# Kernel optimization log

Measured on AMD Instinct MI355X. Metric: run time of the kernel, lower is better.

The kernel has to match this reference:

```python
import jax, jax.numpy as jnp
import numpy as np
import math

DIM = 512
HEADS = 8
K_SEEDS = 4
HEAD_DIM = DIM // HEADS
EPS = 1e-6


def setup_inputs() -> dict:
    key = jax.random.key(0)
    ks = jax.random.split(key, 12)
    B, N = 16, 8192
    s = 1.0 / math.sqrt(DIM)
    inp = {
        "X": jax.random.normal(ks[0], (B, N, DIM), dtype=jnp.float32),
        "seed": jax.random.normal(ks[1], (1, K_SEEDS, DIM), dtype=jnp.float32),
        "Wq": jax.random.uniform(ks[2], (DIM, DIM), minval=-s, maxval=s),
        "bq": jax.random.uniform(ks[3], (DIM,), minval=-s, maxval=s),
        "Wk": jax.random.uniform(ks[4], (DIM, DIM), minval=-s, maxval=s),
        "bk": jax.random.uniform(ks[5], (DIM,), minval=-s, maxval=s),
        "Wv": jax.random.uniform(ks[6], (DIM, DIM), minval=-s, maxval=s),
        "bv": jax.random.uniform(ks[7], (DIM,), minval=-s, maxval=s),
        "Wo": jax.random.uniform(ks[8], (DIM, DIM), minval=-s, maxval=s),
        "bo": jax.random.uniform(ks[9], (DIM,), minval=-s, maxval=s),
        "gamma": jnp.ones((DIM,), dtype=jnp.float32),
        "beta": jnp.zeros((DIM,), dtype=jnp.float32),
    }
    return inp


def reference(X, seed, Wq, bq, Wk, bk, Wv, bv, Wo, bo, gamma, beta):
    B, N, _ = X.shape
    S = jnp.broadcast_to(seed, (B, K_SEEDS, DIM))  # expanded seed vectors
    # QKV projections (torch Linear: x @ W.T + b)
    q = (S @ Wq.T + bq).reshape(B, K_SEEDS, HEADS, HEAD_DIM)
    k = (X @ Wk.T + bk).reshape(B, N, HEADS, HEAD_DIM)
    v = (X @ Wv.T + bv).reshape(B, N, HEADS, HEAD_DIM)
    # scores: [B, H, Kq, N]
    scores = jnp.einsum("bqhd,bnhd->bhqn", q, k) / math.sqrt(HEAD_DIM)
    attn = jax.nn.softmax(scores, axis=-1)
    out = jnp.einsum("bhqn,bnhd->bqhd", attn, v).reshape(B, K_SEEDS, DIM)
    out = out @ Wo.T + bo
    # residual + LayerNorm
    h = out + S
    mu = jnp.mean(h, axis=-1, keepdims=True)
    var = jnp.mean((h - mu) ** 2, axis=-1, keepdims=True)
    return (h - mu) * jax.lax.rsqrt(var + EPS) * gamma + beta
```

## Files before the change

kernel.cpp:

```cpp
#include <hip/hip_runtime.h>
#include <math.h>

#define DIM 512
#define KQn 4
#define HQ  32
#define BB  16
#define NN  8192
#define EPSLN 1e-6f
#define TROWS  32

typedef _Float16 f16;
typedef _Float16 h2_t __attribute__((ext_vector_type(2)));
typedef __fp16   g2_t __attribute__((ext_vector_type(2)));
typedef _Float16 h8_t __attribute__((ext_vector_type(8)));
typedef float    f32x4 __attribute__((ext_vector_type(4)));

union U32H2 { unsigned int u; h2_t h; g2_t g; };
union U4H8  { uint4 u; h8_t h; unsigned int w[4]; };

__device__ inline unsigned int pkh2(float a, float b) {
    U32H2 v; v.g = __builtin_amdgcn_cvt_pkrtz(a, b); return v.u;
}
__device__ inline h2_t ash2(unsigned int u) { U32H2 v; v.u = u; return v.h; }

#if __has_builtin(__builtin_amdgcn_fdot2)
__device__ inline float fdot2f(unsigned int a, unsigned int b, float c) {
    return __builtin_amdgcn_fdot2(ash2(a), ash2(b), c, false);
}
#else
__device__ inline float fdot2f(unsigned int a, unsigned int b, float c) {
    h2_t ha = ash2(a), hb = ash2(b);
    return c + (float)ha.x*(float)hb.x + (float)ha.y*(float)hb.y;
}
#endif

__global__ __launch_bounds__(256) void k_q(
    const float* __restrict__ seed, const float* __restrict__ Wq,
    const float* __restrict__ bq, float* __restrict__ q_g)
{
    int hq = blockIdx.x; int h = hq >> 2; int j = hq & 3;
    int t = threadIdx.x;
    __shared__ float qpart[256];
    int d = t >> 2, q4 = t & 3;
    const float* sr = seed + j*DIM + q4*128;
    const float* wr = Wq + (size_t)(h*64 + d)*DIM + q4*128;
    float acc = 0.f;
    for (int c = 0; c < 128; c += 4) {
        float4 s4 = *(const float4*)(sr + c);
        float4 w4 = *(const float4*)(wr + c);
        acc += s4.x*w4.x + s4.y*w4.y + s4.z*w4.z + s4.w*w4.w;
    }
    qpart[t] = acc;
    __syncthreads();
    if (t < 64)
        q_g[hq*64 + t] = qpart[t*4] + qpart[t*4+1] + qpart[t*4+2] + qpart[t*4+3] + bq[h*64 + t];
}

__global__ __launch_bounds__(256) void k_qk(
    const float* __restrict__ Wk, const float* __restrict__ q_g, f16* __restrict__ qkB)
{
    const int h = blockIdx.x;
    const int cs = blockIdx.y;
    const int t = threadIdx.x;
    __shared__ float q_s[4][64];
    __shared__ float red2[4][128];
    q_s[t >> 6][t & 63] = q_g[(h*4 + (t >> 6))*64 + (t & 63)];
    __syncthreads();
    const int c = cs*128 + (t & 127);
    const int dh = t >> 7;
    float a0=0.f, a1=0.f, a2=0.f, a3=0.f;
    const float* wb = Wk + ((size_t)(h*64 + dh*32))*DIM + c;
    #pragma unroll 8
    for (int d = 0; d < 32; ++d) {
        float w = wb[(size_t)d*DIM];
        a0 += q_s[0][dh*32 + d]*w;
        a1 += q_s[1][dh*32 + d]*w;
        a2 += q_s[2][dh*32 + d]*w;
        a3 += q_s[3][dh*32 + d]*w;
    }
    if (dh == 1) {
        red2[0][t & 127] = a0; red2[1][t & 127] = a1;
        red2[2][t & 127] = a2; red2[3][t & 127] = a3;
    }
    __syncthreads();
    if (dh == 0) {
        int ci = t & 127;
        float v[4];
        v[0] = (a0 + red2[0][ci]) * 0.125f;
        v[1] = (a1 + red2[1][ci]) * 0.125f;
        v[2] = (a2 + red2[2][ci]) * 0.125f;
        v[3] = (a3 + red2[3][ci]) * 0.125f;
        const int kb = c >> 5, g = (c >> 3) & 3, ii = c & 7;
        #pragma unroll
        for (int j = 0; j < 4; ++j) {
            const int hq = h*4 + j;
            const int nb = hq >> 4, lane = g*16 + (hq & 15);
            qkB[(((size_t)(kb*2 + nb)*64 + lane) << 3) + ii] = (f16)v[j];
        }
    }
}

__global__ __launch_bounds__(256, 4) void k_att(
    const float* __restrict__ X, const f16* __restrict__ qkB,
    f16* __restrict__ opart, float* __restrict__ lpart,
    int nchunk, int crows, int ntile)
{
    const int chunk = blockIdx.x, b = blockIdx.y;
    const int t = threadIdx.x;

    __shared__ f16 Xcm[512][36];
    __shared__ f16 p_s[32][36];
    __shared__ float lred[256];

    unsigned int* XcmU = (unsigned int*)&Xcm[0][0];
    unsigned int* pW   = (unsigned int*)&p_s[0][0];

    const int w    = t >> 6;
    const int lane = t & 63;
    const int mb = w & 1, nb = w >> 1;
    const int lg = lane >> 4;
    const int lm = lane & 15;

    const int rp = t >> 4;
    const int cq = (t & 15) << 1;

    const int hg = t >> 5;
    const int cg = t & 31;

    float o_acc[4][16];
    #pragma unroll
    for (int j = 0; j < 4; ++j)
        #pragma unroll
        for (int i = 0; i < 16; ++i) o_acc[j][i] = 0.f;
    float l_local = 0.f;

    const size_t xbase = (size_t)b*NN*DIM;
    const uint4* qkB4 = (const uint4*)qkB;

    for (int tile = 0; tile < ntile; ++tile) {
        const int r0 = chunk*crows + tile*TROWS;
        __syncthreads();
        {
            const float2* Xr0 = (const float2*)(X + xbase + (size_t)(r0 + rp*2    )*DIM);
            const float2* Xr1 = (const float2*)(X + xbase + (size_t)(r0 + rp*2 + 1)*DIM);
            #pragma unroll
            for (int cs = 0; cs < 16; ++cs) {
                int c0 = cs*32 + cq;
                float2 xa = Xr0[c0 >> 1];
                float2 xb = Xr1[c0 >> 1];
                XcmU[c0*18 + rp]     = pkh2(xa.x, xb.x);
                XcmU[(c0+1)*18 + rp] = pkh2(xa.y, xb.y);
            }
        }
        {
            const float* xr = X + xbase + (size_t)(r0 + mb*16 + lm)*DIM + lg*8;
            f32x4 acc0 = {0.f,0.f,0.f,0.f}, acc1 = {0.f,0.f,0.f,0.f};
            #pragma unroll
            for (int kb = 0; kb < 16; ++kb) {
                float4 a0 = *(const float4*)(xr + kb*32);
                float4 a1 = *(const float4*)(xr + kb*32 + 4);
                U4H8 af;
                af.w[0] = pkh2(a0.x, a0.y); af.w[1] = pkh2(a0.z, a0.w);
                af.w[2] = pkh2(a1.x, a1.y); af.w[3] = pkh2(a1.z, a1.w);
                U4H8 bf; bf.u = qkB4[(size_t)(kb*2 + nb)*64 + lane];
                if (kb & 1) acc1 = __builtin_amdgcn_mfma_f32_16x16x32_f16(af.h, bf.h, acc1, 0, 0, 0);
                else        acc0 = __builtin_amdgcn_mfma_f32_16x16x32_f16(af.h, bf.h, acc0, 0, 0, 0);
            }
            float p0 = __expf(fminf(acc0[0] + acc1[0], 30.f));
            float p1 = __expf(fminf(acc0[1] + acc1[1], 30.f));
            float p2 = __expf(fminf(acc0[2] + acc1[2], 30.f));
            float p3 = __expf(fminf(acc0[3] + acc1[3], 30.f));
            l_local += p0 + p1 + p2 + p3;
            const int pidx = (nb*16 + lm)*18 + mb*8 + lg*2;
            pW[pidx]     = pkh2(p0, p1);
            pW[pidx + 1] = pkh2(p2, p3);
        }
        __syncthreads();
        {
            const unsigned int* pU = (const unsigned int*)&p_s[0][0];
            #pragma unroll
            for (int ng = 0; ng < 4; ++ng) {
                unsigned int pd[4][4];
                #pragma unroll
                for (int j = 0; j < 4; ++j) {
                    uint2 pa = *(const uint2*)&pU[(hg*4 + j)*18 + ng*4];
                    uint2 pb = *(const uint2*)&pU[(hg*4 + j)*18 + ng*4 + 2];
                    pd[j][0] = pa.x; pd[j][1] = pa.y; pd[j][2] = pb.x; pd[j][3] = pb.y;
                }
                #pragma unroll
                for (int mm = 0; mm < 4; ++mm) {
                    #pragma unroll
                    for (int cc = 0; cc < 4; ++cc) {
                        const int c = cg + mm*32 + cc*128;
                        const int ci = mm*4 + cc;
                        const unsigned int* row = &XcmU[c*18 + ng*4];
                        uint2 xa = *(const uint2*)&row[0];
                        uint2 xb = *(const uint2*)&row[2];
                        #pragma unroll
                        for (int j = 0; j < 4; ++j) {
                            float a = o_acc[j][ci];
                            a = fdot2f(pd[j][0], xa.x, a);
                            a = fdot2f(pd[j][1], xa.y, a);
                            a = fdot2f(pd[j][2], xb.x, a);
                            a = fdot2f(pd[j][3], xb.y, a);
                            o_acc[j][ci] = a;
                        }
                    }
                }
            }
        }
    }
    __syncthreads();
    lred[w*64 + lane] = l_local;
    __syncthreads();
    if (t < 32) {
        const int nb2 = t >> 4, col = t & 15;
        float l = 0.f;
        #pragma unroll
        for (int mm = 0; mm < 2; ++mm)
            #pragma unroll
            for (int g = 0; g < 4; ++g)
                l += lred[(nb2*2 + mm)*64 + g*16 + col];
        lpart[((size_t)b*nchunk + chunk)*HQ + t] = l;
    }
    const size_t obase = (((size_t)b*nchunk + chunk)*HQ + hg*4)*DIM + cg;
    #pragma unroll
    for (int j = 0; j < 4; ++j)
        #pragma unroll
        for (int mm = 0; mm < 4; ++mm)
            #pragma unroll
            for (int cc = 0; cc < 4; ++cc)
                opart[obase + (size_t)j*DIM + mm*32 + cc*128] = (f16)o_acc[j][mm*4 + cc];
}

__global__ __launch_bounds__(256) void k_red(
    const f16* __restrict__ opart, const float* __restrict__ lpart,
    const float* __restrict__ Wv, const float* __restrict__ bv,
    float* __restrict__ vbuf, int nchunk)
{
    const int hq = blockIdx.x, b = blockIdx.y;
    const int h = hq >> 2, j = hq & 3;
    const int t = threadIdx.x;
    __shared__ float pool_s[512];
    __shared__ float ls[64];
    __shared__ float linv_s;
    if (t < nchunk) ls[t] = lpart[((size_t)b*nchunk + t)*HQ + hq];
    __syncthreads();
    if (t == 0) {
        float l = 0.f;
        for (int i = 0; i < nchunk; ++i) l += ls[i];
        linv_s = 1.f / l;
    }
    float a0 = 0.f, a1 = 0.f;
    const unsigned int* opU = (const unsigned int*)opart;
    #pragma unroll 4
    for (int ch = 0; ch < nchunk; ++ch) {
        unsigned int u = opU[((((size_t)b*nchunk + ch)*HQ + hq) << 8) + t];
        h2_t hv = ash2(u);
        a0 += (float)hv.x; a1 += (float)hv.y;
    }
    __syncthreads();
    float linv = linv_s;
    pool_s[2*t]   = a0 * linv;
    pool_s[2*t+1] = a1 * linv;
    __syncthreads();
    const int o1 = t >> 2, q4 = t & 3;
    const float* wr = Wv + ((size_t)(h*64 + o1))*DIM + q4*128;
    const float* ps = pool_s + q4*128;
    float acc = 0.f;
    #pragma unroll 8
    for (int c = 0; c < 128; c += 4) {
        float4 w4 = *(const float4*)(wr + c);
        float4 p4 = *(const float4*)(ps + c);
        acc += w4.x*p4.x + w4.y*p4.y + w4.z*p4.z + w4.w*p4.w;
    }
    acc += __shfl_xor(acc, 1);
    acc += __shfl_xor(acc, 2);
    if (q4 == 0)
        vbuf[((size_t)b*KQn + j)*DIM + h*64 + o1] = acc + bv[h*64 + o1];
}

__global__ __launch_bounds__(512) void k_wo_ln(
    const float* __restrict__ vbuf, const float* __restrict__ Wo, const float* __restrict__ bo,
    const float* __restrict__ seed, const float* __restrict__ gamma, const float* __restrict__ beta,
    float* __restrict__ out)
{
    const int j = blockIdx.x, b = blockIdx.y;
    const int t = threadIdx.x;
    __shared__ float v_s[512];
    __shared__ float wsum[8], wsq[8];
    v_s[t] = vbuf[((size_t)b*KQn + j)*DIM + t];
    __syncthreads();
    const float* wr = Wo + (size_t)t*DIM;
    float acc = bo[t];
    #pragma unroll 8
    for (int c = 0; c < 512; c += 4) {
        float4 w4 = *(const float4*)(wr + c);
        float4 p4 = *(const float4*)&v_s[c];
        acc += w4.x*p4.x + w4.y*p4.y + w4.z*p4.z + w4.w*p4.w;
    }
    float hv = acc + seed[j*DIM + t];
    float s1 = hv, s2 = hv*hv;
    #pragma unroll
    for (int m = 1; m <= 32; m <<= 1) {
        s1 += __shfl_xor(s1, m);
        s2 += __shfl_xor(s2, m);
    }
    if ((t & 63) == 0) { wsum[t >> 6] = s1; wsq[t >> 6] = s2; }
    __syncthreads();
    float tm = 0.f, tq = 0.f;
    #pragma unroll
    for (int i = 0; i < 8; ++i) { tm += wsum[i]; tq += wsq[i]; }
    float mu = tm * (1.f/512.f);
    float var = tq * (1.f/512.f) - mu*mu;
    float rs = rsqrtf(var + EPSLN);
    out[((size_t)b*KQn + j)*DIM + t] = (hv - mu)*rs*gamma[t] + beta[t];
}

extern "C" void kernel_launch(void* const* d_in, const int* in_sizes, int n_in,
                              void* d_out, int out_size, void* d_ws, size_t ws_size,
                              hipStream_t stream) {
    const float* X     = (const float*)d_in[0];
    const float* seed  = (const float*)d_in[1];
    const float* Wq    = (const float*)d_in[2];
    const float* bq    = (const float*)d_in[3];
    const float* Wk    = (const float*)d_in[4];
    const float* Wv    = (const float*)d_in[6];
    const float* bv    = (const float*)d_in[7];
    const float* Wo    = (const float*)d_in[8];
    const float* bo    = (const float*)d_in[9];
    const float* gamma = (const float*)d_in[10];
    const float* beta  = (const float*)d_in[11];

    int nchunk = 64;
    {
        const size_t need64 = 303104UL + (size_t)BB*64*HQ*DIM*2;
        if (ws_size < need64) nchunk = 32;
    }
    const int crows = NN / nchunk;
    const int ntile = crows / TROWS;

    char* ws = (char*)d_ws;
    float* q_g   = (float*)(ws + 0);
    f16*   qkB   = (f16*)  (ws + 8192);
    size_t off_lpart = 40960;
    size_t off_vbuf  = off_lpart + (size_t)BB*nchunk*HQ*4;
    size_t off_opart = off_vbuf + (size_t)BB*KQn*DIM*4;
    float* lpart = (float*)(ws + off_lpart);
    float* vbuf  = (float*)(ws + off_vbuf);
    f16*   opart = (f16*)  (ws + off_opart);
    float* out   = (float*)d_out;

    k_q    <<<32,               256, 0, stream>>>(seed, Wq, bq, q_g);
    k_qk   <<<dim3(8, 4),       256, 0, stream>>>(Wk, q_g, qkB);
    k_att  <<<dim3(nchunk, BB), 256, 0, stream>>>(X, qkB, opart, lpart, nchunk, crows, ntile);
    k_red  <<<dim3(HQ, BB),     256, 0, stream>>>(opart, lpart, Wv, bv, vbuf, nchunk);
    k_wo_ln<<<dim3(KQn, BB),    512, 0, stream>>>(vbuf, Wo, bo, seed, gamma, beta, out);
}
```

Measured before the change: 555.7 us.

## Use MFMA for attention-weighted X accumulation instead of fdot2 loops

Replaces the scalar fdot2-based P·X accumulation in k_att with 16x16x32 f16 MFMA instructions, reading P fragments from a re-padded shared buffer and X column-major fragments from Xcm. Partial outputs are staged through shared memory and written out with coalesced 16-byte stores instead of scattered f16 stores. k_red's chunk-sum of the softmax denominators becomes a wavefront shuffle reduction instead of a serial loop. This should cut the VALU work in the main loop, in exchange for more complex fragment indexing and extra LDS traffic for the output transpose.

```diff
diff --git a/kernel.cpp b/kernel.cpp
--- a/kernel.cpp
+++ b/kernel.cpp
@@ -22,17 +22,6 @@
     U32H2 v; v.g = __builtin_amdgcn_cvt_pkrtz(a, b); return v.u;
 }
 __device__ inline h2_t ash2(unsigned int u) { U32H2 v; v.u = u; return v.h; }
-
-#if __has_builtin(__builtin_amdgcn_fdot2)
-__device__ inline float fdot2f(unsigned int a, unsigned int b, float c) {
-    return __builtin_amdgcn_fdot2(ash2(a), ash2(b), c, false);
-}
-#else
-__device__ inline float fdot2f(unsigned int a, unsigned int b, float c) {
-    h2_t ha = ash2(a), hb = ash2(b);
-    return c + (float)ha.x*(float)hb.x + (float)ha.y*(float)hb.y;
-}
-#endif
 
 __global__ __launch_bounds__(256) void k_q(
     const float* __restrict__ seed, const float* __restrict__ Wq,
@@ -109,7 +98,7 @@
     const int t = threadIdx.x;
 
     __shared__ f16 Xcm[512][36];
-    __shared__ f16 p_s[32][36];
+    __shared__ f16 p_s[32][40];
     __shared__ float lred[256];
 
     unsigned int* XcmU = (unsigned int*)&Xcm[0][0];
@@ -124,14 +113,13 @@
     const int rp = t >> 4;
     const int cq = (t & 15) << 1;
 
-    const int hg = t >> 5;
-    const int cg = t & 31;
-
-    float o_acc[4][16];
+    f32x4 o_acc[8][2];
     #pragma unroll
-    for (int j = 0; j < 4; ++j)
-        #pragma unroll
-        for (int i = 0; i < 16; ++i) o_acc[j][i] = 0.f;
+    for (int cb = 0; cb < 8; ++cb) {
+        #pragma unroll
+        for (int hb = 0; hb < 2; ++hb)
+            o_acc[cb][hb] = (f32x4){0.f,0.f,0.f,0.f};
+    }
     float l_local = 0.f;
 
     const size_t xbase = (size_t)b*NN*DIM;
@@ -171,47 +159,42 @@
             float p2 = __expf(fminf(acc0[2] + acc1[2], 30.f));
             float p3 = __expf(fminf(acc0[3] + acc1[3], 30.f));
             l_local += p0 + p1 + p2 + p3;
-            const int pidx = (nb*16 + lm)*18 + mb*8 + lg*2;
+            const int pidx = (nb*16 + lm)*20 + mb*8 + lg*2;
             pW[pidx]     = pkh2(p0, p1);
             pW[pidx + 1] = pkh2(p2, p3);
         }
         __syncthreads();
         {
-            const unsigned int* pU = (const unsigned int*)&p_s[0][0];
+            U4H8 bf0, bf1;
+            const int pbase = lm*20 + lg*4;
+            bf0.u = *(const uint4*)&pW[pbase];
+            bf1.u = *(const uint4*)&pW[320 + pbase];
             #pragma unroll
-            for (int ng = 0; ng < 4; ++ng) {
-                unsigned int pd[4][4];
-                #pragma unroll
-                for (int j = 0; j < 4; ++j) {
-                    uint2 pa = *(const uint2*)&pU[(hg*4 + j)*18 + ng*4];
-                    uint2 pb = *(const uint2*)&pU[(hg*4 + j)*18 + ng*4 + 2];
-                    pd[j][0] = pa.x; pd[j][1] = pa.y; pd[j][2] = pb.x; pd[j][3] = pb.y;
-                }
-                #pragma unroll
-                for (int mm = 0; mm < 4; ++mm) {
-                    #pragma unroll
-                    for (int cc = 0; cc < 4; ++cc) {
-                        const int c = cg + mm*32 + cc*128;
-                        const int ci = mm*4 + cc;
-                        const unsigned int* row = &XcmU[c*18 + ng*4];
-                        uint2 xa = *(const uint2*)&row[0];
-                        uint2 xb = *(const uint2*)&row[2];
-                        #pragma unroll
-                        for (int j = 0; j < 4; ++j) {
-                            float a = o_acc[j][ci];
-                            a = fdot2f(pd[j][0], xa.x, a);
-                            a = fdot2f(pd[j][1], xa.y, a);
-                            a = fdot2f(pd[j][2], xb.x, a);
-                            a = fdot2f(pd[j][3], xb.y, a);
-                            o_acc[j][ci] = a;
-                        }
-                    }
-                }
+            for (int cb = 0; cb < 8; ++cb) {
+                const int c = (w*8 + cb)*16 + lm;
+                const unsigned int* row = &XcmU[c*18 + lg*4];
+                uint2 xa = *(const uint2*)&row[0];
+                uint2 xb = *(const uint2*)&row[2];
+                U4H8 af;
+                af.w[0] = xa.x; af.w[1] = xa.y; af.w[2] = xb.x; af.w[3] = xb.y;
+                o_acc[cb][0] = __builtin_amdgcn_mfma_f32_16x16x32_f16(af.h, bf0.h, o_acc[cb][0], 0, 0, 0);
+                o_acc[cb][1] = __builtin_amdgcn_mfma_f32_16x16x32_f16(af.h, bf1.h, o_acc[cb][1], 0, 0, 0);
             }
         }
     }
     __syncthreads();
-    lred[w*64 + lane] = l_local;
+    lred[t] = l_local;
+    unsigned int* otU = (unsigned int*)&Xcm[0][0];
+    #pragma unroll
+    for (int cb = 0; cb < 8; ++cb) {
+        const int chalf = ((w*8 + cb)*16 + lg*4) >> 1;
+        #pragma unroll
+        for (int hb = 0; hb < 2; ++hb) {
+            const int hq = hb*16 + lm;
+            otU[hq*260 + chalf]     = pkh2(o_acc[cb][hb][0], o_acc[cb][hb][1]);
+            otU[hq*260 + chalf + 1] = pkh2(o_acc[cb][hb][2], o_acc[cb][hb][3]);
+        }
+    }
     __syncthreads();
     if (t < 32) {
         const int nb2 = t >> 4, col = t & 15;
@@ -223,14 +206,14 @@
                 l += lred[(nb2*2 + mm)*64 + g*16 + col];
         lpart[((size_t)b*nchunk + chunk)*HQ + t] = l;
     }
-    const size_t obase = (((size_t)b*nchunk + chunk)*HQ + hg*4)*DIM + cg;
-    #pragma unroll
-    for (int j = 0; j < 4; ++j)
-        #pragma unroll
-        for (int mm = 0; mm < 4; ++mm)
-            #pragma unroll
-            for (int cc = 0; cc < 4; ++cc)
-                opart[obase + (size_t)j*DIM + mm*32 + cc*128] = (f16)o_acc[j][mm*4 + cc];
+    {
+        const int hq_w = t >> 3, c0 = (t & 7) << 6;
+        const unsigned int* src = &otU[hq_w*260 + (c0 >> 1)];
+        f16* dst = opart + (((size_t)b*nchunk + chunk)*HQ + hq_w)*DIM + c0;
+        #pragma unroll
+        for (int i = 0; i < 4; ++i)
+            *(uint4*)(dst + i*16) = *(const uint4*)(src + i*8);
+    }
 }
 
 __global__ __launch_bounds__(256) void k_red(
@@ -242,14 +225,12 @@
     const int h = hq >> 2, j = hq & 3;
     const int t = threadIdx.x;
     __shared__ float pool_s[512];
-    __shared__ float ls[64];
     __shared__ float linv_s;
-    if (t < nchunk) ls[t] = lpart[((size_t)b*nchunk + t)*HQ + hq];
-    __syncthreads();
-    if (t == 0) {
-        float l = 0.f;
-        for (int i = 0; i < nchunk; ++i) l += ls[i];
-        linv_s = 1.f / l;
+    if (t < 64) {
+        float l = (t < nchunk) ? lpart[((size_t)b*nchunk + t)*HQ + hq] : 0.f;
+        #pragma unroll
+        for (int m = 1; m < 64; m <<= 1) l += __shfl_xor(l, m);
+        if (t == 0) linv_s = 1.f / l;
     }
     float a0 = 0.f, a1 = 0.f;
     const unsigned int* opU = (const unsigned int*)opart;
```

Result: faster. 536.5 us (-3.5%).
